# Performance work log

Hardware: AMD Instinct MI355X
Metric: run time of the kernel (lower is better)

The kernel has to match this reference:

```python
import jax, jax.numpy as jnp
import numpy as np

B, S, DIM = 16, 8192, 128
H, KV, D = 4, 2, 64  # heads, kv_heads, dim_head


def setup_inputs() -> dict:
    key = jax.random.key(0)
    ks = jax.random.split(key, 8)
    scale = 0.05
    return {
        "x": jax.random.normal(ks[0], (B, S, DIM), dtype=jnp.float32),
        "Wq": jax.random.normal(ks[1], (H, D, DIM), dtype=jnp.float32) * scale,
        "bq": jax.random.normal(ks[2], (H, D), dtype=jnp.float32) * scale,
        "Wk": jax.random.normal(ks[3], (KV, D, DIM), dtype=jnp.float32) * scale,
        "bk": jax.random.normal(ks[4], (KV, D), dtype=jnp.float32) * scale,
        "Wv": jax.random.normal(ks[5], (KV, D, DIM), dtype=jnp.float32) * scale,
        "bv": jax.random.normal(ks[6], (KV, D), dtype=jnp.float32) * scale,
        "Wo": jax.random.normal(ks[7], (DIM, DIM), dtype=jnp.float32) * scale,
    }


def reference(x, Wq, bq, Wk, bk, Wv, bv, Wo):
    b, s, _ = x.shape
    # MultiHeadLinear: per-head Linear stacked on last axis -> [B,S,D,H]
    q_st = jnp.einsum("bsc,hdc->bsdh", x, Wq) + bq.T  # [B,S,D,H]
    k_st = jnp.einsum("bsc,hdc->bsdh", x, Wk) + bk.T  # [B,S,D,KV]
    v_st = jnp.einsum("bsc,hdc->bsdh", x, Wv) + bv.T  # [B,S,D,KV]
    # .view(B,-1,heads,dim_head): raw reshape of (D,H) block into (H,D)
    q = q_st.reshape(b, s, H, D)
    k = k_st.reshape(b, s, KV, D)
    v = v_st.reshape(b, s, KV, D)
    # k scaled by q mean over heads (no softmax anywhere)
    k = k * jnp.mean(q, axis=2, keepdims=True)  # [B,S,KV,D]
    attn = jnp.einsum("bshd,bskd->bshk", q, k) / jnp.sqrt(jnp.asarray(D, q.dtype))
    out = jnp.einsum("bshk,bskd->bshd", attn, v)  # [B,S,H,D]
    # reshape(B,-1,dim): [B,S,H*D=256] -> [B,2S,128]
    out = out.reshape(b, -1, DIM)
    return out @ Wo.T
```

## Files before the change

### kernel.cpp

```cpp
#include <hip/hip_runtime.h>
#include <stdint.h>


using short8 = __attribute__((ext_vector_type(8))) short;
using f32x4  = __attribute__((ext_vector_type(4))) float;
using f32x2  = __attribute__((ext_vector_type(2))) float;

constexpr int XSTR = 136;
constexpr int PSTR = 10;
constexpr int T_TILES = 8;

__device__ __forceinline__ unsigned short f2bf(float f) {
    unsigned int u = __float_as_uint(f);
    u += 0x7FFFu + ((u >> 16) & 1u);
    return (unsigned short)(u >> 16);
}

__device__ __forceinline__ void barrier_nodrain() {
    asm volatile("s_waitcnt lgkmcnt(0)\n\ts_barrier" ::: "memory");
}

__global__ void prep_weights(const float* __restrict__ Wq, const float* __restrict__ bq,
                             const float* __restrict__ Wk, const float* __restrict__ bk,
                             const float* __restrict__ Wv, const float* __restrict__ bv,
                             const float* __restrict__ Wo,
                             unsigned short* __restrict__ Wp, float* __restrict__ bias)
{
    const int ch = blockIdx.x;
    const int c  = threadIdx.x;
    float w, b;
    if (ch < 256) {
        const int hh = ch & 3, dd = ch >> 2;
        w = Wq[(hh * 64 + dd) * 128 + c];
        b = bq[hh * 64 + dd];
    } else if (ch < 384) {
        const int i = ch - 256;
        const int kvh = i & 1, dd = i >> 1;
        w = Wk[(kvh * 64 + dd) * 128 + c];
        b = bk[kvh * 64 + dd];
    } else {
        const int i  = ch - 384;
        const int jg = i >> 6, kp = (i >> 4) & 3, jm = i & 15;
        const int j  = (jg >> 1) * 32 + jm * 2 + (jg & 1);
        const int kv = kp >> 1, p = kp & 1;
        float acc = 0.f, bacc = 0.f;
        #pragma unroll 8
        for (int d = 0; d < 64; ++d) {
            const int idx = kv * 64 + d;
            const int kvh = idx & 1, dd = idx >> 1;
            const float wo = Wo[j * 128 + p * 64 + d];
            acc  += wo * Wv[(kvh * 64 + dd) * 128 + c];
            bacc += wo * bv[kvh * 64 + dd];
        }
        w = acc; b = bacc;
    }
    Wp[ch * 128 + c] = f2bf(w);
    if (c == 0) bias[ch] = b;
}

__device__ __forceinline__ void stage8_load(const float* __restrict__ x, int tb, int row0,
                                            int l, float4* xv)
{
    const int row = row0 + (l >> 3);
    const float* src = x + (size_t)(tb + row) * 128 + (l & 7) * 4;
    #pragma unroll
    for (int j = 0; j < 4; ++j) xv[j] = *(const float4*)(src + 32 * j);
}
__device__ __forceinline__ void stage8_write(unsigned short* __restrict__ xb, int row0,
                                             int l, const float4* xv)
{
    const int row = row0 + (l >> 3);
    #pragma unroll
    for (int j = 0; j < 4; ++j) {
        ushort4 s;
        s.x = f2bf(xv[j].x); s.y = f2bf(xv[j].y); s.z = f2bf(xv[j].z); s.w = f2bf(xv[j].w);
        *(ushort4*)&xb[row * XSTR + (l & 7) * 4 + 32 * j] = s;
    }
}

__global__ __launch_bounds__(512, 1)
void fused_attn_kernel(const float* __restrict__ x,
                       const unsigned short* __restrict__ Wp,
                       const float* __restrict__ bias,
                       float* __restrict__ out)
{
    __shared__ __align__(16) unsigned short xlds[3][64 * XSTR];
    __shared__ __align__(16) float partial[2][4][64][PSTR];
    __shared__ __align__(16) float coeffw[4][64][8];

    const int tid = threadIdx.x;
    const int l   = tid & 63;
    const int wv  = tid >> 6;
    const int lr  = l & 15, lg = l >> 4;
    const int tok0 = blockIdx.x * (T_TILES * 64);

    if (wv < 4) {
        const int dc   = wv;
        const int row0 = wv * 16;
        int chb[6];
        #pragma unroll
        for (int n = 0; n < 4; ++n) chb[n] = n * 64 + dc * 16;
        chb[4] = 256 + dc * 16;
        chb[5] = 320 + dc * 16;

        short8 areg[24];
        #pragma unroll
        for (int n = 0; n < 6; ++n)
            #pragma unroll
            for (int ks = 0; ks < 4; ++ks)
                areg[n * 4 + ks] = *(const short8*)(Wp + (size_t)(chb[n] + lr) * 128 + ks * 32 + lg * 8);
        f32x4 biasv[6];
        #pragma unroll
        for (int n = 0; n < 6; ++n)
            biasv[n] = *(const f32x4*)(bias + chb[n] + lg * 4);

        auto phase1 = [&](const unsigned short* __restrict__ xb, int pb) {
            #pragma unroll
            for (int p = 0; p < 4; ++p) {
                f32x4 acc[6];
                #pragma unroll
                for (int n = 0; n < 6; ++n) acc[n] = (f32x4){0.f, 0.f, 0.f, 0.f};
                #pragma unroll
                for (int ks = 0; ks < 4; ++ks) {
                    short8 bfr = *(const short8*)&xb[(p * 16 + lr) * XSTR + ks * 32 + lg * 8];
                    #pragma unroll
                    for (int n = 0; n < 6; ++n)
                        acc[n] = __builtin_amdgcn_mfma_f32_16x16x32_bf16(
                            areg[n * 4 + ks], bfr, acc[n], 0, 0, 0);
                }
                float pa[8];
                #pragma unroll
                for (int c = 0; c < 8; ++c) pa[c] = 0.f;
                #pragma unroll
                for (int r = 0; r < 4; ++r) {
                    const float q0 = acc[0][r] + biasv[0][r];
                    const float q1 = acc[1][r] + biasv[1][r];
                    const float q2 = acc[2][r] + biasv[2][r];
                    const float q3 = acc[3][r] + biasv[3][r];
                    const float k0v = acc[4][r] + biasv[4][r];
                    const float k1v = acc[5][r] + biasv[5][r];
                    const float qm  = 0.25f * (q0 + q1 + q2 + q3);
                    const float kt0 = k0v * qm, kt1 = k1v * qm;
                    pa[0] += q0 * kt0; pa[1] += q1 * kt0;
                    pa[2] += q0 * kt1; pa[3] += q1 * kt1;
                    pa[4] += q2 * kt0; pa[5] += q3 * kt0;
                    pa[6] += q2 * kt1; pa[7] += q3 * kt1;
                }
                #pragma unroll
                for (int c = 0; c < 8; ++c) pa[c] += __shfl_xor(pa[c], 16);
                #pragma unroll
                for (int c = 0; c < 8; ++c) pa[c] += __shfl_xor(pa[c], 32);
                if (lg == 0) {
                    float* dst = &partial[pb][dc][p * 16 + lr][0];
                    *(float2*)(dst)     = make_float2(pa[0], pa[1]);
                    *(float2*)(dst + 2) = make_float2(pa[2], pa[3]);
                    *(float2*)(dst + 4) = make_float2(pa[4], pa[5]);
                    *(float2*)(dst + 6) = make_float2(pa[6], pa[7]);
                }
            }
        };

        float4 xa[4], xb_[4];
        stage8_load(x, tok0, row0,     l, xa);
        stage8_load(x, tok0, row0 + 8, l, xb_);
        stage8_write(xlds[0], row0,     l, xa);
        stage8_write(xlds[0], row0 + 8, l, xb_);
        barrier_nodrain();
        stage8_load(x, tok0 + 64, row0,     l, xa);
        stage8_load(x, tok0 + 64, row0 + 8, l, xb_);
        phase1(xlds[0], 0);
        stage8_write(xlds[1], row0,     l, xa);
        stage8_write(xlds[1], row0 + 8, l, xb_);
        barrier_nodrain();

        for (int t = 0; t < T_TILES; ++t) {
            const bool do_stage = (t < T_TILES - 2);
            if (do_stage) {
                stage8_load(x, tok0 + (t + 2) * 64, row0,     l, xa);
                stage8_load(x, tok0 + (t + 2) * 64, row0 + 8, l, xb_);
            }
            if (t < T_TILES - 1) phase1(xlds[(t + 1) % 3], (t + 1) & 1);
            if (do_stage) {
                stage8_write(xlds[(t + 2) % 3], row0,     l, xa);
                stage8_write(xlds[(t + 2) % 3], row0 + 8, l, xb_);
            }
            barrier_nodrain();
        }
    } else {
        const int jgp = wv - 4;

        short8 breg[32];
        #pragma unroll
        for (int j2 = 0; j2 < 2; ++j2)
            #pragma unroll
            for (int kp = 0; kp < 4; ++kp)
                #pragma unroll
                for (int ks = 0; ks < 4; ++ks)
                    breg[(j2 * 4 + kp) * 4 + ks] = *(const short8*)
                        (Wp + (size_t)(384 + (jgp * 2 + j2) * 64 + kp * 16 + lr) * 128 + ks * 32 + lg * 8);
        float bvv[2][4];
        #pragma unroll
        for (int j2 = 0; j2 < 2; ++j2)
            #pragma unroll
            for (int kp = 0; kp < 4; ++kp)
                bvv[j2][kp] = bias[384 + (jgp * 2 + j2) * 64 + kp * 16 + lr];

        barrier_nodrain();
        barrier_nodrain();

        for (int t = 0; t < T_TILES; ++t) {
            {
                const int pb = t & 1;
                float s[8];
                #pragma unroll
                for (int c = 0; c < 8; ++c) s[c] = 0.f;
                #pragma unroll
                for (int dcc = 0; dcc < 4; ++dcc) {
                    const float* pr = &partial[pb][dcc][l][0];
                    #pragma unroll
                    for (int c = 0; c < 4; ++c) {
                        float2 v = *(const float2*)(pr + 2 * c);
                        s[2 * c] += v.x; s[2 * c + 1] += v.y;
                    }
                }
                float* cw = &coeffw[jgp][l][0];
                *(float2*)(cw)     = make_float2(s[0] * 0.125f, s[1] * 0.125f);
                *(float2*)(cw + 2) = make_float2(s[2] * 0.125f, s[3] * 0.125f);
                *(float2*)(cw + 4) = make_float2(s[4] * 0.125f, s[5] * 0.125f);
                *(float2*)(cw + 6) = make_float2(s[6] * 0.125f, s[7] * 0.125f);
            }

            {
                const unsigned short* xb = xlds[t % 3];
                const int g0    = tok0 + t * 64;
                const int bb    = g0 >> 13;
                const int srow0 = bb * 16384 + 2 * (g0 & 8191);
                #pragma unroll
                for (int mf = 0; mf < 4; ++mf) {
                    f32x4 a2[2][4];
                    #pragma unroll
                    for (int j2 = 0; j2 < 2; ++j2)
                        #pragma unroll
                        for (int kp = 0; kp < 4; ++kp)
                            a2[j2][kp] = (f32x4){0.f, 0.f, 0.f, 0.f};
                    #pragma unroll
                    for (int ks = 0; ks < 4; ++ks) {
                        short8 af = *(const short8*)&xb[(mf * 16 + lr) * XSTR + ks * 32 + lg * 8];
                        #pragma unroll
                        for (int j2 = 0; j2 < 2; ++j2)
                            #pragma unroll
                            for (int kp = 0; kp < 4; ++kp)
                                a2[j2][kp] = __builtin_amdgcn_mfma_f32_16x16x32_bf16(
                                    af, breg[(j2 * 4 + kp) * 4 + ks], a2[j2][kp], 0, 0, 0);
                    }
                    #pragma unroll
                    for (int r = 0; r < 4; ++r) {
                        const int tokL = lg * 4 + r;
                        const int tok  = mf * 16 + tokL;
                        f32x4 cl = *(const f32x4*)&coeffw[jgp][tok][0];
                        f32x4 ch = *(const f32x4*)&coeffw[jgp][tok][4];
                        f32x2 s0, s1;
                        {
                            const float a0 = a2[0][0][r] + bvv[0][0];
                            const float a1 = a2[0][1][r] + bvv[0][1];
                            const float av = a2[0][2][r] + bvv[0][2];
                            const float a3 = a2[0][3][r] + bvv[0][3];
                            s0[0] = cl[0] * a0 + cl[1] * a1 + cl[2] * av + cl[3] * a3;
                            s1[0] = ch[0] * a0 + ch[1] * a1 + ch[2] * av + ch[3] * a3;
                        }
                        {
                            const float a0 = a2[1][0][r] + bvv[1][0];
                            const float a1 = a2[1][1][r] + bvv[1][1];
                            const float av = a2[1][2][r] + bvv[1][2];
                            const float a3 = a2[1][3][r] + bvv[1][3];
                            s0[1] = cl[0] * a0 + cl[1] * a1 + cl[2] * av + cl[3] * a3;
                            s1[1] = ch[0] * a0 + ch[1] * a1 + ch[2] * av + ch[3] * a3;
                        }
                        const int row = srow0 + 32 * mf + 2 * tokL;
                        float* dst = out + (size_t)row * 128 + jgp * 32 + lr * 2;
                        __builtin_nontemporal_store(s0, (f32x2*)(dst));
                        __builtin_nontemporal_store(s1, (f32x2*)(dst + 128));
                    }
                }
            }
            barrier_nodrain();
        }
    }
}

extern "C" void kernel_launch(void* const* d_in, const int* in_sizes, int n_in,
                              void* d_out, int out_size, void* d_ws, size_t ws_size,
                              hipStream_t stream)
{
    (void)in_sizes; (void)n_in; (void)out_size; (void)ws_size;
    const float* x  = (const float*)d_in[0];
    const float* Wq = (const float*)d_in[1];
    const float* bq = (const float*)d_in[2];
    const float* Wk = (const float*)d_in[3];
    const float* bk = (const float*)d_in[4];
    const float* Wv = (const float*)d_in[5];
    const float* bv = (const float*)d_in[6];
    const float* Wo = (const float*)d_in[7];

    unsigned short* Wp   = (unsigned short*)d_ws;
    float*          bias = (float*)((char*)d_ws + 896 * 128 * 2);

    prep_weights<<<896, 128, 0, stream>>>(Wq, bq, Wk, bk, Wv, bv, Wo, Wp, bias);
    fused_attn_kernel<<<256, 512, 0, stream>>>(x, Wp, bias, (float*)d_out);
}
```

Baseline: 56.15 us.

## Replace block barriers with LDS flag spin-waits and add fourth x buffer

Replaces the per-tile s_barrier between producer waves (QK projection) and consumer waves (V projection and output) with LDS atomic counters and spin-waits. Producers can now run ahead of consumers using a 4-deep x staging ring. Adds s_setprio around the MFMA loops so matrix work gets scheduling priority. The intent is to remove lock-step stalls between the two wave groups. Spinning on volatile LDS costs issue slots and risks subtle ordering bugs.

```diff
diff --git a/kernel.cpp b/kernel.cpp
--- a/kernel.cpp
+++ b/kernel.cpp
@@ -16,8 +16,12 @@
     return (unsigned short)(u >> 16);
 }
 
-__device__ __forceinline__ void barrier_nodrain() {
-    asm volatile("s_waitcnt lgkmcnt(0)\n\ts_barrier" ::: "memory");
+__device__ __forceinline__ void lds_fence() {
+    asm volatile("s_waitcnt lgkmcnt(0)" ::: "memory");
+}
+__device__ __forceinline__ void spin_ge(const volatile int* f, int v) {
+    while (*f < v) { }
+    asm volatile("" ::: "memory");
 }
 
 __global__ void prep_weights(const float* __restrict__ Wq, const float* __restrict__ bq,
@@ -84,9 +88,13 @@
                        const float* __restrict__ bias,
                        float* __restrict__ out)
 {
-    __shared__ __align__(16) unsigned short xlds[3][64 * XSTR];
+    __shared__ __align__(16) unsigned short xlds[4][64 * XSTR];
     __shared__ __align__(16) float partial[2][4][64][PSTR];
     __shared__ __align__(16) float coeffw[4][64][8];
+    __shared__ int flg_xready[T_TILES];
+    __shared__ int flg_xdone [T_TILES];
+    __shared__ int flg_pready[T_TILES];
+    __shared__ int flg_pdone [T_TILES];
 
     const int tid = threadIdx.x;
     const int l   = tid & 63;
@@ -94,6 +102,12 @@
     const int lr  = l & 15, lg = l >> 4;
     const int tok0 = blockIdx.x * (T_TILES * 64);
 
+    if (tid < T_TILES) {
+        flg_xready[tid] = 0; flg_xdone[tid] = 0;
+        flg_pready[tid] = 0; flg_pdone[tid] = 0;
+    }
+    __syncthreads();
+
     if (wv < 4) {
         const int dc   = wv;
         const int row0 = wv * 16;
@@ -120,6 +134,7 @@
                 f32x4 acc[6];
                 #pragma unroll
                 for (int n = 0; n < 6; ++n) acc[n] = (f32x4){0.f, 0.f, 0.f, 0.f};
+                __builtin_amdgcn_s_setprio(1);
                 #pragma unroll
                 for (int ks = 0; ks < 4; ++ks) {
                     short8 bfr = *(const short8*)&xb[(p * 16 + lr) * XSTR + ks * 32 + lg * 8];
@@ -128,6 +143,7 @@
                         acc[n] = __builtin_amdgcn_mfma_f32_16x16x32_bf16(
                             areg[n * 4 + ks], bfr, acc[n], 0, 0, 0);
                 }
+                __builtin_amdgcn_s_setprio(0);
                 float pa[8];
                 #pragma unroll
                 for (int c = 0; c < 8; ++c) pa[c] = 0.f;
@@ -160,31 +176,44 @@
             }
         };
 
-        float4 xa[4], xb_[4];
-        stage8_load(x, tok0, row0,     l, xa);
-        stage8_load(x, tok0, row0 + 8, l, xb_);
-        stage8_write(xlds[0], row0,     l, xa);
-        stage8_write(xlds[0], row0 + 8, l, xb_);
-        barrier_nodrain();
-        stage8_load(x, tok0 + 64, row0,     l, xa);
-        stage8_load(x, tok0 + 64, row0 + 8, l, xb_);
-        phase1(xlds[0], 0);
-        stage8_write(xlds[1], row0,     l, xa);
-        stage8_write(xlds[1], row0 + 8, l, xb_);
-        barrier_nodrain();
-
-        for (int t = 0; t < T_TILES; ++t) {
-            const bool do_stage = (t < T_TILES - 2);
+        {
+            float4 xa[4], xb_[4];
+            stage8_load(x, tok0, row0,     l, xa);
+            stage8_load(x, tok0, row0 + 8, l, xb_);
+            stage8_write(xlds[0], row0,     l, xa);
+            stage8_write(xlds[0], row0 + 8, l, xb_);
+            lds_fence();
+            if (l == 0) atomicAdd(&flg_xready[0], 1);
+            stage8_load(x, tok0 + 64, row0,     l, xa);
+            stage8_load(x, tok0 + 64, row0 + 8, l, xb_);
+            stage8_write(xlds[1], row0,     l, xa);
+            stage8_write(xlds[1], row0 + 8, l, xb_);
+            lds_fence();
+            if (l == 0) atomicAdd(&flg_xready[1], 1);
+        }
+
+        for (int u = 0; u < T_TILES; ++u) {
+            float4 xa[4], xb_[4];
+            const bool do_stage = (u + 2 < T_TILES);
             if (do_stage) {
-                stage8_load(x, tok0 + (t + 2) * 64, row0,     l, xa);
-                stage8_load(x, tok0 + (t + 2) * 64, row0 + 8, l, xb_);
-            }
-            if (t < T_TILES - 1) phase1(xlds[(t + 1) % 3], (t + 1) & 1);
+                stage8_load(x, tok0 + (u + 2) * 64, row0,     l, xa);
+                stage8_load(x, tok0 + (u + 2) * 64, row0 + 8, l, xb_);
+            }
+            if (u >= 2) spin_ge(&flg_pdone[u - 2], 4);
+            spin_ge(&flg_xready[u], 4);
+            phase1(xlds[u & 3], u & 1);
+            lds_fence();
+            if (l == 0) {
+                atomicAdd(&flg_pready[u], 1);
+                atomicAdd(&flg_xdone[u], 1);
+            }
             if (do_stage) {
-                stage8_write(xlds[(t + 2) % 3], row0,     l, xa);
-                stage8_write(xlds[(t + 2) % 3], row0 + 8, l, xb_);
-            }
-            barrier_nodrain();
+                if (u >= 2) spin_ge(&flg_xdone[u - 2], 8);
+                stage8_write(xlds[(u + 2) & 3], row0,     l, xa);
+                stage8_write(xlds[(u + 2) & 3], row0 + 8, l, xb_);
+                lds_fence();
+                if (l == 0) atomicAdd(&flg_xready[u + 2], 1);
+            }
         }
     } else {
         const int jgp = wv - 4;
@@ -205,10 +234,8 @@
             for (int kp = 0; kp < 4; ++kp)
                 bvv[j2][kp] = bias[384 + (jgp * 2 + j2) * 64 + kp * 16 + lr];
 
-        barrier_nodrain();
-        barrier_nodrain();
-
         for (int t = 0; t < T_TILES; ++t) {
+            spin_ge(&flg_pready[t], 4);
             {
                 const int pb = t & 1;
                 float s[8];
@@ -229,9 +256,12 @@
                 *(float2*)(cw + 4) = make_float2(s[4] * 0.125f, s[5] * 0.125f);
                 *(float2*)(cw + 6) = make_float2(s[6] * 0.125f, s[7] * 0.125f);
             }
-
+            lds_fence();
+            if (l == 0) atomicAdd(&flg_pdone[t], 1);
+
+            spin_ge(&flg_xready[t], 4);
             {
-                const unsigned short* xb = xlds[t % 3];
+                const unsigned short* xb = xlds[t & 3];
                 const int g0    = tok0 + t * 64;
                 const int bb    = g0 >> 13;
                 const int srow0 = bb * 16384 + 2 * (g0 & 8191);
@@ -243,6 +273,7 @@
                         #pragma unroll
                         for (int kp = 0; kp < 4; ++kp)
                             a2[j2][kp] = (f32x4){0.f, 0.f, 0.f, 0.f};
+                    __builtin_amdgcn_s_setprio(1);
                     #pragma unroll
                     for (int ks = 0; ks < 4; ++ks) {
                         short8 af = *(const short8*)&xb[(mf * 16 + lr) * XSTR + ks * 32 + lg * 8];
@@ -253,6 +284,7 @@
                                 a2[j2][kp] = __builtin_amdgcn_mfma_f32_16x16x32_bf16(
                                     af, breg[(j2 * 4 + kp) * 4 + ks], a2[j2][kp], 0, 0, 0);
                     }
+                    __builtin_amdgcn_s_setprio(0);
                     #pragma unroll
                     for (int r = 0; r < 4; ++r) {
                         const int tokL = lg * 4 + r;
@@ -283,7 +315,8 @@
                     }
                 }
             }
-            barrier_nodrain();
+            lds_fence();
+            if (l == 0) atomicAdd(&flg_xdone[t], 1);
         }
     }
 }
```

Result: no change. 55.75 us (-0.7%).
